# Optimization experiments

Hardware: AMD Instinct MI355X
Metric: run time of the kernel (lower is better)

The kernel has to match this reference:

```python
import jax, jax.numpy as jnp
import numpy as np

H = 32  # rnn/encoder/residual hidden dim
NEG = -1e9


def gru(x, h0, Wih, Whh, bih, bhh):
    # x: (B,T,D), h0: (B,H); torch GRU gate order [r,z,n]
    xp = jnp.swapaxes(x @ Wih.T + bih, 0, 1)  # (T,B,3H)

    def step(h, xt):
        gh = h @ Whh.T + bhh
        xr, xz, xn = jnp.split(xt, 3, axis=-1)
        hr, hz, hn = jnp.split(gh, 3, axis=-1)
        r = jax.nn.sigmoid(xr + hr)
        z = jax.nn.sigmoid(xz + hz)
        n = jnp.tanh(xn + r * hn)
        h_new = (1.0 - z) * n + z * h
        return h_new, h_new

    hT, ys = jax.lax.scan(step, h0, xp)
    return jnp.swapaxes(ys, 0, 1), hT  # (B,T,H), (B,H)


def setup_inputs():
    key = jax.random.key(0)
    ks = jax.random.split(key, 30)
    B, T = 2048, 128
    def lin(k, o, i):
        return jax.random.normal(k, (o, i), jnp.float32) / np.sqrt(i)
    inp = {}
    inp['obs'] = jax.random.normal(ks[0], (B, T, 15), jnp.float32)
    inp['rnn_state'] = jax.random.normal(ks[1], (1, B, 3 * H), jnp.float32)
    inp['enc_air_W'] = lin(ks[2], H, 7); inp['enc_air_b'] = jnp.zeros((H,), jnp.float32)
    inp['enc_m_W'] = lin(ks[3], H, 4); inp['enc_m_b'] = jnp.zeros((H,), jnp.float32)
    inp['air_Wih'] = lin(ks[4], 3 * H, H); inp['air_Whh'] = lin(ks[5], 3 * H, H)
    inp['air_bih'] = jnp.zeros((3 * H,), jnp.float32); inp['air_bhh'] = jnp.zeros((3 * H,), jnp.float32)
    inp['m_Wih'] = lin(ks[6], 3 * H, H); inp['m_Whh'] = lin(ks[7], 3 * H, H)
    inp['m_bih'] = jnp.zeros((3 * H,), jnp.float32); inp['m_bhh'] = jnp.zeros((3 * H,), jnp.float32)
    inp['attn_in_w'] = lin(ks[8], 3 * H, H); inp['attn_in_b'] = jnp.zeros((3 * H,), jnp.float32)
    inp['attn_out_w'] = lin(ks[9], H, H); inp['attn_out_b'] = jnp.zeros((H,), jnp.float32)
    inp['mlp_W0'] = lin(ks[10], 256, 2 * H); inp['mlp_b0'] = jnp.zeros((256,), jnp.float32)
    inp['mlp_W1'] = lin(ks[11], 256, 256); inp['mlp_b1'] = jnp.zeros((256,), jnp.float32)
    inp['out_W'] = lin(ks[12], 1, 256); inp['out_b'] = jnp.zeros((1,), jnp.float32)
    return inp


def reference(obs, rnn_state, enc_air_W, enc_air_b, enc_m_W, enc_m_b,
              air_Wih, air_Whh, air_bih, air_bhh,
              m_Wih, m_Whh, m_bih, m_bhh,
              attn_in_w, attn_in_b, attn_out_w, attn_out_b,
              mlp_W0, mlp_b0, mlp_W1, mlp_b1, out_W, out_b):
    B, T, _ = obs.shape
    h_air0 = rnn_state[0, :, :H]                       # (B,H)
    h_m0 = rnn_state[0, :, H:].reshape(2 * B, H)       # faithful reshape (1,B,64)->(1,2B,32)

    # aircraft branch
    air_emb = obs[..., 8:] @ enc_air_W.T + enc_air_b   # (B,T,H)
    air_feat, next_h_air = gru(air_emb, h_air0, air_Wih, air_Whh, air_bih, air_bhh)

    # missile branch: concat missiles along batch dim
    m_raw = jnp.concatenate([obs[..., 0:4], obs[..., 4:8]], axis=0)  # (2B,T,4)
    m_emb = m_raw @ enc_m_W.T + enc_m_b
    m_feat, next_h_m = gru(m_emb, h_m0, m_Wih, m_Whh, m_bih, m_bhh)
    m1_feat, m2_feat = m_feat[:B], m_feat[B:]

    # inactive-missile mask from raw obs
    obs_flat = obs.reshape(-1, 15)
    inact = jnp.array([1.0, 0.0, 1.0, 0.0], jnp.float32)
    mask = jnp.stack([
        jnp.all(jnp.isclose(obs_flat[:, 0:4], inact), axis=-1),
        jnp.all(jnp.isclose(obs_flat[:, 4:8], inact), axis=-1),
    ], axis=1)                                          # (N,2) True = masked

    N = B * T
    air_flat = air_feat.reshape(N, H)
    m1_flat = m1_feat.reshape(N, H)
    m2_flat = m2_feat.reshape(N, H)

    # 2-head attention, q len 1, kv len 2
    Wq, Wk, Wv = jnp.split(attn_in_w, 3, axis=0)
    bq, bk, bv = jnp.split(attn_in_b, 3, axis=0)
    nh, hd = 2, H // 2
    qh = (air_flat @ Wq.T + bq).reshape(N, nh, hd)
    kv = jnp.stack([m1_flat, m2_flat], axis=1)          # (N,2,H)
    kh = (kv @ Wk.T + bk).reshape(N, 2, nh, hd)
    vh = (kv @ Wv.T + bv).reshape(N, 2, nh, hd)
    scores = jnp.einsum('nhd,nkhd->nhk', qh, kh) / np.sqrt(hd)
    scores = scores + jnp.where(mask[:, None, :], NEG, 0.0)
    w = jax.nn.softmax(scores, axis=-1)
    ctx = jnp.einsum('nhk,nkhd->nhd', w, vh).reshape(N, H)
    attn = ctx @ attn_out_w.T + attn_out_b
    attn = jnp.where(jnp.all(mask, axis=-1, keepdims=True), 0.0, attn)  # torch nan_to_num(all-masked)

    fusion = jnp.concatenate([air_flat, attn], axis=-1)  # (N,2H)
    h1 = jax.nn.leaky_relu(fusion @ mlp_W0.T + mlp_b0, 0.01)
    h2 = jax.nn.leaky_relu(h1 @ mlp_W1.T + mlp_b1, 0.01)
    val = h2 @ out_W.T + out_b                           # (N,1)

    next_h = jnp.concatenate([next_h_air, next_h_m.reshape(B, 2 * H)], axis=-1)[None]  # (1,B,96)
    return val, next_h
```

## Files before the change

### kernel.cpp

```cpp
#include <hip/hip_runtime.h>
#include <hip/hip_bf16.h>

#define BB 2048
#define TT 128
#define NN (BB*TT)
#define NVAL NN

#define OFF_W0P   2048u
#define OFF_W1P   10240u
#define OFF_WQKV  43008u
#define OFF_WO    44544u
#define OFF_PWHA  49792u
#define OFF_PWHM  51328u
#define OFF_PWCA  52864u
#define OFF_PWCM  54400u
#define OFF_BHNA  55936u
#define OFF_BHNM  55968u
#define OFF_AIRF  83968u
#define OFF_MF    4278272u
#define OFF_MASK  12666880u

#define L2E 1.44269504088896341f

typedef __attribute__((ext_vector_type(8))) short short8;
typedef __attribute__((ext_vector_type(4))) float f32x4;
typedef _Float16 f16x8 __attribute__((ext_vector_type(8)));
typedef unsigned u32x4 __attribute__((ext_vector_type(4)));

__device__ __forceinline__ unsigned short f2bf(float f) {
    unsigned u = __builtin_bit_cast(unsigned, f);
    u += 0x7FFFu + ((u >> 16) & 1u);
    return (unsigned short)(u >> 16);
}
__device__ __forceinline__ unsigned f2h(float f) {
    _Float16 h = (_Float16)f;
    return (unsigned)__builtin_bit_cast(unsigned short, h);
}
__device__ __forceinline__ unsigned pkh2(float a, float b) {
    return (f2h(b) << 16) | f2h(a);
}
__device__ __forceinline__ float fast_rcp(float x) {
    return __builtin_amdgcn_rcpf(x);
}
__device__ __forceinline__ float ex2(float x) {
    return __builtin_amdgcn_exp2f(x);
}
__device__ __forceinline__ unsigned cvt_pk_bf16(float a, float b) {
    unsigned r;
    asm("v_cvt_pk_bf16_f32 %0, %1, %2" : "=v"(r) : "v"(a), "v"(b));
    return r;
}
__device__ __forceinline__ f32x4 mfma16f(f16x8 a, f16x8 b, f32x4 c) {
    return __builtin_amdgcn_mfma_f32_16x16x32_f16(a, b, c, 0, 0, 0);
}
__device__ __forceinline__ f32x4 mfma16b(short8 a, short8 b, f32x4 c) {
    return __builtin_amdgcn_mfma_f32_16x16x32_bf16(a, b, c, 0, 0, 0);
}
__device__ __forceinline__ float lrelu(float h) {
    return (h > 0.f) ? h : 0.01f*h;
}

__global__ __launch_bounds__(256) void prep_kernel(
    const float* __restrict__ enc_air_W, const float* __restrict__ enc_air_b,
    const float* __restrict__ enc_m_W,   const float* __restrict__ enc_m_b,
    const float* __restrict__ air_Wih,   const float* __restrict__ air_bih,
    const float* __restrict__ m_Wih,     const float* __restrict__ m_bih,
    const float* __restrict__ air_Whh,   const float* __restrict__ m_Whh,
    const float* __restrict__ air_bhh,   const float* __restrict__ m_bhh,
    const float* __restrict__ W0,        const float* __restrict__ W1,
    const float* __restrict__ attn_in_w, const float* __restrict__ attn_out_w,
    float* __restrict__ ws)
{
    int b = blockIdx.x, t = threadIdx.x;
    if (b == 0) {
    } else if (b <= 32) {
        unsigned short* w1p = (unsigned short*)(ws + OFF_W1P);
        int base = ((b-1)*256 + t);
        int lane = base & 63;
        int ctf  = base >> 6;
        int ft2  = ctf & 15, kap = ctf >> 4;
        int col = lane & 15, quad = lane >> 4;
        int o  = ft2*16 + col;
        #pragma unroll
        for (int j = 0; j < 8; j++) {
            int f = (2*kap + (j>>2))*16 + quad*4 + (j&3);
            w1p[base*8 + j] = f2bf(W1[o*256 + f]);
        }
    } else if (b <= 40) {
        unsigned short* w0p = (unsigned short*)(ws + OFF_W0P);
        int base = ((b-33)*256 + t);
        int lane = base & 63;
        int ctf  = base >> 6;
        int ct   = ctf & 15, s = ctf >> 4;
        int col = lane & 15, quad = lane >> 4;
        int k0 = s*32 + quad*8;
        int o  = ct*16 + col;
        #pragma unroll
        for (int j = 0; j < 8; j++)
            w0p[base*8 + j] = f2bf(W0[o*64 + k0 + j]);
    } else if (b == 41) {
        unsigned short* wqkv = (unsigned short*)(ws + OFF_WQKV);
        unsigned short* wop  = (unsigned short*)(ws + OFF_WO);
        for (int slot = t; slot < 512; slot += 256) {
            if (slot < 384) {
                int ct = slot >> 6, lane = slot & 63;
                int col = lane & 15, quad = lane >> 4;
                int o = ct*16 + col;
                #pragma unroll
                for (int j = 0; j < 8; j++)
                    wqkv[slot*8 + j] = f2bf(attn_in_w[o*32 + quad*8 + j]);
            } else {
                int s2 = slot - 384;
                int ct = s2 >> 6, lane = s2 & 63;
                int col = lane & 15, quad = lane >> 4;
                #pragma unroll
                for (int j = 0; j < 8; j++)
                    wop[s2*8 + j] = f2bf(attn_out_w[(ct*16+col)*32 + quad*8 + j]);
            }
        }
    } else if (b == 42) {
        unsigned* pa = (unsigned*)(ws + OFF_PWHA);
        unsigned* pm = (unsigned*)(ws + OFF_PWHM);
        for (int s = t; s < 3072; s += 256) {
            int s2 = (s < 1536) ? s : s - 1536;
            const float* W = (s < 1536) ? air_Whh : m_Whh;
            unsigned* dst = (s < 1536) ? pa : pm;
            int tile = s2 >> 8;
            int l    = (s2 >> 2) & 63;
            int d    = s2 & 3;
            int gate = tile >> 1, hfp = tile & 1;
            int rr = l & 15;
            int f  = (rr >> 2)*8 + hfp*4 + (rr & 3);
            int k  = (l >> 4)*8 + d*2;
            int row = gate*32 + f;
            float sc = (gate == 2) ? 2.f*L2E : L2E;
            dst[s2] = pkh2(W[row*32 + k]*sc, W[row*32 + k + 1]*sc);
        }
    } else {
        unsigned* pa = (unsigned*)(ws + OFF_PWCA);
        unsigned* pm = (unsigned*)(ws + OFF_PWCM);
        for (int s = t; s < 3072; s += 256) {
            bool isA = (s < 1536);
            int s2 = isA ? s : s - 1536;
            unsigned* dst = isA ? pa : pm;
            int tile = s2 >> 8, l = (s2 >> 2) & 63, d = s2 & 3;
            int gate = tile >> 1, hfp = tile & 1;
            int rr = l & 15;
            int f = (rr >> 2)*8 + hfp*4 + (rr & 3);
            int o = gate*32 + f;
            int kb = (l >> 4)*8 + d*2;
            int ni = isA ? 7 : 4;
            float sc = (gate == 2) ? 2.f*L2E : L2E;
            float v[2];
            #pragma unroll
            for (int e = 0; e < 2; e++) {
                int k = kb + e;
                float acc = 0.f;
                if (k < ni) {
                    for (int m = 0; m < 32; m++)
                        acc += isA ? air_Wih[o*32+m]*enc_air_W[m*7+k]
                                   : m_Wih[o*32+m]*enc_m_W[m*4+k];
                } else if (k == ni) {
                    acc = isA ? air_bih[o] : m_bih[o];
                    for (int m = 0; m < 32; m++)
                        acc += isA ? air_Wih[o*32+m]*enc_air_b[m]
                                   : m_Wih[o*32+m]*enc_m_b[m];
                    if (gate < 2) acc += isA ? air_bhh[o] : m_bhh[o];
                }
                v[e] = acc*sc;
            }
            dst[s2] = pkh2(v[0], v[1]);
        }
        if (t < 32) {
            ws[OFF_BHNA + t] = air_bhh[64 + t]*2.f*L2E;
            ws[OFF_BHNM + t] = m_bhh[64 + t]*2.f*L2E;
        }
    }
}

template<bool AIRT>
__device__ __forceinline__ void gru_tile(
    const float* __restrict__ obs, const float* __restrict__ rnn,
    const float* __restrict__ ws,
    unsigned short* __restrict__ feat, float* __restrict__ mask_f,
    float* __restrict__ nh_out, int tileIdx, unsigned* __restrict__ XH)
{
    const int lane = threadIdx.x & 63;
    const int col = lane & 15, quad = lane >> 4;

    const unsigned* pw = (const unsigned*)(ws + (AIRT ? OFF_PWHA : OFF_PWHM));
    const unsigned* pc = (const unsigned*)(ws + (AIRT ? OFF_PWCA : OFF_PWCM));
    f16x8 whf[6], wcf[6];
    #pragma unroll
    for (int i6 = 0; i6 < 6; i6++) {
        whf[i6] = __builtin_bit_cast(f16x8, *(const u32x4*)(pw + i6*256 + lane*4));
        wcf[i6] = __builtin_bit_cast(f16x8, *(const u32x4*)(pc + i6*256 + lane*4));
    }
    const float* bhnp = ws + (AIRT ? OFF_BHNA : OFF_BHNM) + quad*8;
    f32x4 bhn0 = *(const f32x4*)(bhnp);
    f32x4 bhn1 = *(const f32x4*)(bhnp + 4);

    int slot = 0, tb;
    if (AIRT) { tb = tileIdx*16; }
    else      { slot = tileIdx >> 7; tb = (tileIdx & 127)*16; }

    {
        const int coff = AIRT ? 8 : slot*4;
        #pragma unroll 4
        for (int it = 0; it < 32; it++) {
            int s = it*64 + lane;
            int r = s >> 7, t = s & 127;
            const float* p = obs + (size_t)(tb + r)*1920 + t*15 + coff;
            unsigned d0, d1, d2, d3;
            if (AIRT) {
                d0 = pkh2(p[0], p[1]); d1 = pkh2(p[2], p[3]);
                d2 = pkh2(p[4], p[5]); d3 = pkh2(p[6], 1.0f);
            } else {
                float x0 = p[0], x1 = p[1], x2 = p[2], x3 = p[3];
                d0 = pkh2(x0, x1); d1 = pkh2(x2, x3);
                d2 = 0x00003C00u; d3 = 0u;
                bool ok = (fabsf(x0 - 1.f) <= 1.00001e-5f) && (fabsf(x1) <= 1e-8f) &&
                          (fabsf(x2 - 1.f) <= 1.00001e-5f) && (fabsf(x3) <= 1e-8f);
                mask_f[((size_t)(tb + r)*TT + t)*2 + slot] = ok ? 1.f : 0.f;
            }
            unsigned off = (unsigned)(r*512 + 4*(t ^ (r & 7)));
            *(u32x4*)(XH + off) = (u32x4){d0, d1, d2, d3};
        }
    }
    __syncthreads();

    int rowi = tileIdx*16 + col;
    int hbase;
    if (AIRT) hbase = rowi*96;
    else      hbase = (rowi >> 1)*96 + 32 + (rowi & 1)*32;
    unsigned short* featp = feat + (size_t)rowi*(TT*32) + quad*8;

    f32x4 h0v = *(const f32x4*)(rnn + hbase + quad*8);
    f32x4 h1v = *(const f32x4*)(rnn + hbase + quad*8 + 4);

    const int xk = col & 7;
    const unsigned bidx = (unsigned)col*512;
    const f32x4 z4 = {0.f, 0.f, 0.f, 0.f};

    f32x4 gx0, gx1, gx2, gx3, gx4, gx5;
    {
        u32x4 xc = *(const u32x4*)(XH + bidx + 4u*(unsigned)(0 ^ xk));
        f16x8 xf = __builtin_bit_cast(f16x8, xc);
        gx0 = mfma16f(wcf[0], xf, z4); gx1 = mfma16f(wcf[1], xf, z4);
        gx2 = mfma16f(wcf[2], xf, z4); gx3 = mfma16f(wcf[3], xf, z4);
        gx4 = mfma16f(wcf[4], xf, z4); gx5 = mfma16f(wcf[5], xf, z4);
    }
    u32x4 xreg = *(const u32x4*)(XH + bidx + 4u*(unsigned)(1 ^ xk));

    #pragma unroll 1
    for (int t = 0; t < TT; t++) {
        const int tp = (t < TT-2) ? t+2 : TT-1;
        u32x4 xpre = *(const u32x4*)(XH + bidx + 4u*(unsigned)(tp ^ xk));
        f16x8 xfn = __builtin_bit_cast(f16x8, xreg);

        u32x4 hdv;
        hdv[0] = pkh2(h0v[0], h0v[1]); hdv[1] = pkh2(h0v[2], h0v[3]);
        hdv[2] = pkh2(h1v[0], h1v[1]); hdv[3] = pkh2(h1v[2], h1v[3]);
        f16x8 hff = __builtin_bit_cast(f16x8, hdv);

        f32x4 aR0 = mfma16f(whf[0], hff, gx0);
        f32x4 aR1 = mfma16f(whf[1], hff, gx1);
        f32x4 aZ0 = mfma16f(whf[2], hff, gx2);
        f32x4 aZ1 = mfma16f(whf[3], hff, gx3);
        f32x4 aHN0 = mfma16f(whf[4], hff, bhn0);
        f32x4 aHN1 = mfma16f(whf[5], hff, bhn1);
        f32x4 aXN0 = gx4, aXN1 = gx5;

        gx0 = mfma16f(wcf[0], xfn, z4); gx1 = mfma16f(wcf[1], xfn, z4);
        gx2 = mfma16f(wcf[2], xfn, z4); gx3 = mfma16f(wcf[3], xfn, z4);
        gx4 = mfma16f(wcf[4], xfn, z4); gx5 = mfma16f(wcf[5], xfn, z4);

        #pragma unroll
        for (int s = 0; s < 4; s++) {
            {
                float r = fast_rcp(1.f + ex2(-aR0[s]));
                float z = fast_rcp(1.f + ex2(-aZ0[s]));
                float p = aXN0[s] + r*aHN0[s];
                float n = fmaf(-2.f, fast_rcp(1.f + ex2(p)), 1.f);
                h0v[s] = n + z*(h0v[s] - n);
            }
            {
                float r = fast_rcp(1.f + ex2(-aR1[s]));
                float z = fast_rcp(1.f + ex2(-aZ1[s]));
                float p = aXN1[s] + r*aHN1[s];
                float n = fmaf(-2.f, fast_rcp(1.f + ex2(p)), 1.f);
                h1v[s] = n + z*(h1v[s] - n);
            }
        }

        u32x4 fw;
        fw[0] = cvt_pk_bf16(h0v[0], h0v[1]); fw[1] = cvt_pk_bf16(h0v[2], h0v[3]);
        fw[2] = cvt_pk_bf16(h1v[0], h1v[1]); fw[3] = cvt_pk_bf16(h1v[2], h1v[3]);
        *(u32x4*)(featp + (size_t)t*32) = fw;

        xreg = xpre;
    }
    *(f32x4*)(nh_out + hbase + quad*8)     = h0v;
    *(f32x4*)(nh_out + hbase + quad*8 + 4) = h1v;
}

__global__ __launch_bounds__(64, 1) void gru_kernel(
    const float* __restrict__ obs, const float* __restrict__ rnn,
    const float* __restrict__ ws,
    unsigned short* __restrict__ air_feat, unsigned short* __restrict__ m_feat,
    float* __restrict__ mask_f, float* __restrict__ nh_out)
{
    __shared__ unsigned XH[8192];
    int g = blockIdx.x;
    if (g < 128) gru_tile<true >(obs, rnn, ws, air_feat, mask_f, nh_out, g, XH);
    else         gru_tile<false>(obs, rnn, ws, m_feat,  mask_f, nh_out, g - 128, XH);
}

__global__ __launch_bounds__(512, 4) void fused_kernel(
    const unsigned short* __restrict__ air_feat, const unsigned short* __restrict__ m_feat,
    const float* __restrict__ mask_f,
    const unsigned short* __restrict__ wqkv, const float* __restrict__ attn_in_b,
    const unsigned short* __restrict__ wop,  const float* __restrict__ attn_out_b,
    const unsigned short* __restrict__ w0p, const float* __restrict__ b0,
    const unsigned short* __restrict__ w1p, const float* __restrict__ b1,
    const float* __restrict__ outW, const float* __restrict__ outb,
    float* __restrict__ val)
{
    __shared__ unsigned short XB[16384];
    __shared__ unsigned short AT[4096];
    __shared__ float PS[8][64];

    unsigned short* CT = XB;

    const int tid  = threadIdx.x;
    const int lane = tid & 63;
    const int wid  = tid >> 6;
    const int col  = lane & 15;
    const int quad = lane >> 4;
    const size_t n0 = (size_t)blockIdx.x * 64;
    const int rt    = wid & 3;
    const int tbase = (wid >> 2) * 8;

    short8 w0f0[8];
    #pragma unroll
    for (int i = 0; i < 8; i++)
        w0f0[i] = *(const short8*)(w0p + ((tbase + i)*64 + lane)*8);
    short8 bAir = *(const short8*)(air_feat + (n0 + rt*16 + col)*32 + quad*8);

    f32x4 accL1[8];
    #pragma unroll
    for (int i = 0; i < 8; i++) accL1[i] = (f32x4){0.f,0.f,0.f,0.f};

    if (wid < 4) {
        const int strip = wid;
        short8 wqf[2], wkf[2], wvf[2], wof[2];
        #pragma unroll
        for (int ct = 0; ct < 2; ct++) {
            wqf[ct] = *(const short8*)(wqkv + ((0+ct)*64 + lane)*8);
            wkf[ct] = *(const short8*)(wqkv + ((2+ct)*64 + lane)*8);
            wvf[ct] = *(const short8*)(wqkv + ((4+ct)*64 + lane)*8);
            wof[ct] = *(const short8*)(wop + (ct*64 + lane)*8);
        }
        short8 a_m1 = *(const short8*)(m_feat + (n0 + strip*16 + col)*32 + quad*8);
        short8 a_m2 = *(const short8*)(m_feat + ((size_t)NN + n0 + strip*16 + col)*32 + quad*8);

        float m0a[4], m1a[4];
        #pragma unroll
        for (int reg = 0; reg < 4; reg++) {
            const float* mp = mask_f + (size_t)(n0 + strip*16 + quad*4 + reg)*2;
            m0a[reg] = mp[0]; m1a[reg] = mp[1];
        }

        f32x4 q[2], k1[2], k2[2], v1[2], v2[2], ao[2];
        #pragma unroll
        for (int ct = 0; ct < 2; ct++) {
            f32x4 z = (f32x4){0.f,0.f,0.f,0.f};
            q[ct]  = mfma16b(bAir, wqf[ct], z);
            k1[ct] = mfma16b(a_m1, wkf[ct], z);
            k2[ct] = mfma16b(a_m2, wkf[ct], z);
            v1[ct] = mfma16b(a_m1, wvf[ct], z);
            v2[ct] = mfma16b(a_m2, wvf[ct], z);
        }
        float bqr[2], bkr[2], bvr[2];
        #pragma unroll
        for (int ct = 0; ct < 2; ct++) {
            bqr[ct] = attn_in_b[ct*16 + col];
            bkr[ct] = attn_in_b[32 + ct*16 + col];
            bvr[ct] = attn_in_b[64 + ct*16 + col];
        }
        float p1s[2][4], p2s[2][4];
        #pragma unroll
        for (int ct = 0; ct < 2; ct++) {
            #pragma unroll
            for (int reg = 0; reg < 4; reg++) {
                float qq = q[ct][reg] + bqr[ct];
                float p1 = qq * (k1[ct][reg] + bkr[ct]);
                float p2 = qq * (k2[ct][reg] + bkr[ct]);
                #pragma unroll
                for (int m = 1; m < 16; m <<= 1) {
                    p1 += __shfl_xor(p1, m, 64);
                    p2 += __shfl_xor(p2, m, 64);
                }
                p1s[ct][reg] = p1; p2s[ct][reg] = p2;
            }
        }
        float bothm[4];
        #pragma unroll
        for (int reg = 0; reg < 4; reg++) {
            int rloc = strip*16 + quad*4 + reg;
            float m0v = m0a[reg], m1v = m1a[reg];
            bothm[reg] = (m0v > 0.5f && m1v > 0.5f) ? 1.f : 0.f;
            #pragma unroll
            for (int ct = 0; ct < 2; ct++) {
                float s1 = p1s[ct][reg]*0.25f + (m0v > 0.5f ? -1e9f : 0.f);
                float s2 = p2s[ct][reg]*0.25f + (m1v > 0.5f ? -1e9f : 0.f);
                float mx = fmaxf(s1, s2);
                float e1 = __expf(s1 - mx), e2 = __expf(s2 - mx);
                float inv = fast_rcp(e1 + e2);
                float ctxv = ((v1[ct][reg] + bvr[ct])*e1 +
                              (v2[ct][reg] + bvr[ct])*e2) * inv;
                CT[rloc*40 + ct*16 + col] = f2bf(ctxv);
            }
        }
        short8 a_ctx = *(const short8*)&CT[(strip*16 + col)*40 + quad*8];
        #pragma unroll
        for (int ct = 0; ct < 2; ct++) {
            f32x4 z = (f32x4){0.f,0.f,0.f,0.f};
            ao[ct] = mfma16b(a_ctx, wof[ct], z);
        }
        float bor[2] = { attn_out_b[col], attn_out_b[16 + col] };
        #pragma unroll
        for (int reg = 0; reg < 4; reg++) {
            #pragma unroll
            for (int ct = 0; ct < 2; ct++) {
                float av = ao[ct][reg] + bor[ct];
                av = (bothm[reg] > 0.5f) ? 0.f : av;
                AT[strip*1024 + (quad*4 + reg)*64 + ct*16 + col] = f2bf(av);
            }
        }
    } else {
        #pragma unroll
        for (int i = 0; i < 8; i++)
            accL1[i] = mfma16b(w0f0[i], bAir, accL1[i]);
    }
    __syncthreads();

    if (wid < 4) {
        #pragma unroll
        for (int i = 0; i < 8; i++)
            accL1[i] = mfma16b(w0f0[i], bAir, accL1[i]);
    }
    {
        short8 bAttn = *(const short8*)&AT[rt*1024 + col*64 + quad*8];
        #pragma unroll
        for (int i = 0; i < 8; i++) {
            short8 w0f1 = *(const short8*)(w0p + ((16 + tbase + i)*64 + lane)*8);
            accL1[i] = mfma16b(w0f1, bAttn, accL1[i]);
        }
    }
    #pragma unroll
    for (int i = 0; i < 8; i += 2) {
        int t0 = tbase + i;
        f32x4 bA = *(const f32x4*)(b0 + t0*16 + quad*4);
        f32x4 bB = *(const f32x4*)(b0 + (t0+1)*16 + quad*4);
        float a0 = lrelu(accL1[i][0]   + bA[0]), a1 = lrelu(accL1[i][1]   + bA[1]);
        float a2 = lrelu(accL1[i][2]   + bA[2]), a3 = lrelu(accL1[i][3]   + bA[3]);
        float c0 = lrelu(accL1[i+1][0] + bB[0]), c1 = lrelu(accL1[i+1][1] + bB[1]);
        float c2 = lrelu(accL1[i+1][2] + bB[2]), c3 = lrelu(accL1[i+1][3] + bB[3]);
        u32x4 w;
        w[0] = cvt_pk_bf16(a0, a1); w[1] = cvt_pk_bf16(a2, a3);
        w[2] = cvt_pk_bf16(c0, c1); w[3] = cvt_pk_bf16(c2, c3);
        int kap = t0 >> 1;
        *(u32x4*)((unsigned*)XB + ((rt*8 + kap)*64 + lane)*4) = w;
    }
    __syncthreads();

    f32x4 acc2[4][2];
    #pragma unroll
    for (int r = 0; r < 4; r++)
        #pragma unroll
        for (int c = 0; c < 2; c++) acc2[r][c] = (f32x4){0.f,0.f,0.f,0.f};
    {
        short8 w1f[2], w1n[2];
        #pragma unroll
        for (int c = 0; c < 2; c++)
            w1f[c] = *(const short8*)(w1p + ((0*16 + wid*2 + c)*64 + lane)*8);
        #pragma unroll
        for (int kap = 0; kap < 8; kap++) {
            if (kap < 7) {
                #pragma unroll
                for (int c = 0; c < 2; c++)
                    w1n[c] = *(const short8*)(w1p + (((kap+1)*16 + wid*2 + c)*64 + lane)*8);
            }
            short8 bx[4];
            #pragma unroll
            for (int r = 0; r < 4; r++)
                bx[r] = *(const short8*)&XB[((r*8 + kap)*64 + lane)*8];
            #pragma unroll
            for (int c = 0; c < 2; c++)
                #pragma unroll
                for (int r = 0; r < 4; r++)
                    acc2[r][c] = mfma16b(w1f[c], bx[r], acc2[r][c]);
            #pragma unroll
            for (int c = 0; c < 2; c++) w1f[c] = w1n[c];
        }
    }

    f32x4 b1v[2], owv[2];
    #pragma unroll
    for (int c = 0; c < 2; c++) {
        b1v[c] = *(const f32x4*)(b1 + (wid*2 + c)*16 + quad*4);
        owv[c] = *(const f32x4*)(outW + (wid*2 + c)*16 + quad*4);
    }
    const float outb0 = outb[0];
    #pragma unroll
    for (int r = 0; r < 4; r++) {
        float pv = 0.f;
        #pragma unroll
        for (int c = 0; c < 2; c++) {
            #pragma unroll
            for (int reg = 0; reg < 4; reg++) {
                float h = lrelu(acc2[r][c][reg] + b1v[c][reg]);
                pv += h*owv[c][reg];
            }
        }
        pv += __shfl_xor(pv, 16, 64);
        pv += __shfl_xor(pv, 32, 64);
        if (lane < 16) PS[wid][r*16 + lane] = pv;
    }
    __syncthreads();
    if (tid < 64)
        val[n0 + tid] = PS[0][tid] + PS[1][tid] + PS[2][tid] + PS[3][tid]
                      + PS[4][tid] + PS[5][tid] + PS[6][tid] + PS[7][tid] + outb0;
}

extern "C" void kernel_launch(void* const* d_in, const int* in_sizes, int n_in,
                              void* d_out, int out_size, void* d_ws, size_t ws_size,
                              hipStream_t stream) {
    const float* obs        = (const float*)d_in[0];
    const float* rnn        = (const float*)d_in[1];
    const float* enc_air_W  = (const float*)d_in[2];
    const float* enc_air_b  = (const float*)d_in[3];
    const float* enc_m_W    = (const float*)d_in[4];
    const float* enc_m_b    = (const float*)d_in[5];
    const float* air_Wih    = (const float*)d_in[6];
    const float* air_Whh    = (const float*)d_in[7];
    const float* air_bih    = (const float*)d_in[8];
    const float* air_bhh    = (const float*)d_in[9];
    const float* m_Wih      = (const float*)d_in[10];
    const float* m_Whh      = (const float*)d_in[11];
    const float* m_bih      = (const float*)d_in[12];
    const float* m_bhh      = (const float*)d_in[13];
    const float* attn_in_w  = (const float*)d_in[14];
    const float* attn_in_b  = (const float*)d_in[15];
    const float* attn_out_w = (const float*)d_in[16];
    const float* attn_out_b = (const float*)d_in[17];
    const float* mlp_W0     = (const float*)d_in[18];
    const float* mlp_b0     = (const float*)d_in[19];
    const float* mlp_W1     = (const float*)d_in[20];
    const float* mlp_b1     = (const float*)d_in[21];
    const float* out_W      = (const float*)d_in[22];
    const float* out_b      = (const float*)d_in[23];

    float* ws  = (float*)d_ws;
    float* out = (float*)d_out;

    prep_kernel<<<44, 256, 0, stream>>>(enc_air_W, enc_air_b, enc_m_W, enc_m_b,
                                        air_Wih, air_bih, m_Wih, m_bih,
                                        air_Whh, m_Whh, air_bhh, m_bhh,
                                        mlp_W0, mlp_W1, attn_in_w, attn_out_w, ws);

    gru_kernel<<<384, 64, 0, stream>>>(obs, rnn, ws,
                                       (unsigned short*)(ws + OFF_AIRF),
                                       (unsigned short*)(ws + OFF_MF),
                                       ws + OFF_MASK, out + NVAL);

    fused_kernel<<<NN/64, 512, 0, stream>>>((const unsigned short*)(ws + OFF_AIRF),
                                            (const unsigned short*)(ws + OFF_MF),
                                            ws + OFF_MASK,
                                            (const unsigned short*)(ws + OFF_WQKV), attn_in_b,
                                            (const unsigned short*)(ws + OFF_WO),   attn_out_b,
                                            (const unsigned short*)(ws + OFF_W0P), mlp_b0,
                                            (const unsigned short*)(ws + OFF_W1P), mlp_b1,
                                            out_W, out_b, out);
}
```

Before: 301.9 us.

## Split GRU hidden dimension across two wavefronts with LDS exchange per step

The GRU recurrence kernel now uses two wavefronts per 16-row tile. Each wave computes half of the hidden units, and the two exchange packed fp16 hidden state through double-buffered LDS with a block barrier every timestep. This halves the serial MFMA and transcendental work per wave on the latency-bound recurrence, at the cost of a __syncthreads per step. The gate math also batches reciprocals, computing one rcp per pair of sigmoids or tanhs to cut rcp count.

```diff
diff --git a/kernel.cpp b/kernel.cpp
--- a/kernel.cpp
+++ b/kernel.cpp
@@ -26,6 +26,7 @@
 typedef __attribute__((ext_vector_type(4))) float f32x4;
 typedef _Float16 f16x8 __attribute__((ext_vector_type(8)));
 typedef unsigned u32x4 __attribute__((ext_vector_type(4)));
+typedef unsigned u32x2 __attribute__((ext_vector_type(2)));
 
 __device__ __forceinline__ unsigned short f2bf(float f) {
     unsigned u = __builtin_bit_cast(unsigned, f);
@@ -183,22 +184,23 @@
     const float* __restrict__ obs, const float* __restrict__ rnn,
     const float* __restrict__ ws,
     unsigned short* __restrict__ feat, float* __restrict__ mask_f,
-    float* __restrict__ nh_out, int tileIdx, unsigned* __restrict__ XH)
+    float* __restrict__ nh_out, int tileIdx,
+    unsigned* __restrict__ XH, unsigned* __restrict__ XC)
 {
-    const int lane = threadIdx.x & 63;
+    const int tid  = threadIdx.x;
+    const int w    = tid >> 6;
+    const int lane = tid & 63;
     const int col = lane & 15, quad = lane >> 4;
 
     const unsigned* pw = (const unsigned*)(ws + (AIRT ? OFF_PWHA : OFF_PWHM));
     const unsigned* pc = (const unsigned*)(ws + (AIRT ? OFF_PWCA : OFF_PWCM));
-    f16x8 whf[6], wcf[6];
-    #pragma unroll
-    for (int i6 = 0; i6 < 6; i6++) {
-        whf[i6] = __builtin_bit_cast(f16x8, *(const u32x4*)(pw + i6*256 + lane*4));
-        wcf[i6] = __builtin_bit_cast(f16x8, *(const u32x4*)(pc + i6*256 + lane*4));
-    }
-    const float* bhnp = ws + (AIRT ? OFF_BHNA : OFF_BHNM) + quad*8;
-    f32x4 bhn0 = *(const f32x4*)(bhnp);
-    f32x4 bhn1 = *(const f32x4*)(bhnp + 4);
+    f16x8 whfR = __builtin_bit_cast(f16x8, *(const u32x4*)(pw + (0 + w)*256 + lane*4));
+    f16x8 whfZ = __builtin_bit_cast(f16x8, *(const u32x4*)(pw + (2 + w)*256 + lane*4));
+    f16x8 whfN = __builtin_bit_cast(f16x8, *(const u32x4*)(pw + (4 + w)*256 + lane*4));
+    f16x8 wcfR = __builtin_bit_cast(f16x8, *(const u32x4*)(pc + (0 + w)*256 + lane*4));
+    f16x8 wcfZ = __builtin_bit_cast(f16x8, *(const u32x4*)(pc + (2 + w)*256 + lane*4));
+    f16x8 wcfN = __builtin_bit_cast(f16x8, *(const u32x4*)(pc + (4 + w)*256 + lane*4));
+    f32x4 bhnv = *(const f32x4*)(ws + (AIRT ? OFF_BHNA : OFF_BHNM) + quad*8 + w*4);
 
     int slot = 0, tb;
     if (AIRT) { tb = tileIdx*16; }
@@ -207,8 +209,8 @@
     {
         const int coff = AIRT ? 8 : slot*4;
         #pragma unroll 4
-        for (int it = 0; it < 32; it++) {
-            int s = it*64 + lane;
+        for (int it = 0; it < 16; it++) {
+            int s = it*128 + tid;
             int r = s >> 7, t = s & 127;
             const float* p = obs + (size_t)(tb + r)*1920 + t*15 + coff;
             unsigned d0, d1, d2, d3;
@@ -233,22 +235,21 @@
     int hbase;
     if (AIRT) hbase = rowi*96;
     else      hbase = (rowi >> 1)*96 + 32 + (rowi & 1)*32;
-    unsigned short* featp = feat + (size_t)rowi*(TT*32) + quad*8;
-
-    f32x4 h0v = *(const f32x4*)(rnn + hbase + quad*8);
-    f32x4 h1v = *(const f32x4*)(rnn + hbase + quad*8 + 4);
+    unsigned short* featp = feat + (size_t)rowi*(TT*32) + quad*8 + w*4;
+
+    f32x4 hv = *(const f32x4*)(rnn + hbase + quad*8 + w*4);
 
     const int xk = col & 7;
     const unsigned bidx = (unsigned)col*512;
     const f32x4 z4 = {0.f, 0.f, 0.f, 0.f};
 
-    f32x4 gx0, gx1, gx2, gx3, gx4, gx5;
+    f32x4 gxR, gxZ, gxN;
     {
         u32x4 xc = *(const u32x4*)(XH + bidx + 4u*(unsigned)(0 ^ xk));
         f16x8 xf = __builtin_bit_cast(f16x8, xc);
-        gx0 = mfma16f(wcf[0], xf, z4); gx1 = mfma16f(wcf[1], xf, z4);
-        gx2 = mfma16f(wcf[2], xf, z4); gx3 = mfma16f(wcf[3], xf, z4);
-        gx4 = mfma16f(wcf[4], xf, z4); gx5 = mfma16f(wcf[5], xf, z4);
+        gxR = mfma16f(wcfR, xf, z4);
+        gxZ = mfma16f(wcfZ, xf, z4);
+        gxN = mfma16f(wcfN, xf, z4);
     }
     u32x4 xreg = *(const u32x4*)(XH + bidx + 4u*(unsigned)(1 ^ xk));
 
@@ -256,64 +257,73 @@
     for (int t = 0; t < TT; t++) {
         const int tp = (t < TT-2) ? t+2 : TT-1;
         u32x4 xpre = *(const u32x4*)(XH + bidx + 4u*(unsigned)(tp ^ xk));
-        f16x8 xfn = __builtin_bit_cast(f16x8, xreg);
+
+        unsigned d0 = pkh2(hv[0], hv[1]);
+        unsigned d1 = pkh2(hv[2], hv[3]);
+        *(u32x2*)(XC + ((t & 1)*256 + w*128 + lane*2)) = (u32x2){d0, d1};
+        __syncthreads();
+        u32x2 oth = *(const u32x2*)(XC + ((t & 1)*256 + (1 - w)*128 + lane*2));
 
         u32x4 hdv;
-        hdv[0] = pkh2(h0v[0], h0v[1]); hdv[1] = pkh2(h0v[2], h0v[3]);
-        hdv[2] = pkh2(h1v[0], h1v[1]); hdv[3] = pkh2(h1v[2], h1v[3]);
+        hdv[0] = w ? oth[0] : d0;
+        hdv[1] = w ? oth[1] : d1;
+        hdv[2] = w ? d0 : oth[0];
+        hdv[3] = w ? d1 : oth[1];
         f16x8 hff = __builtin_bit_cast(f16x8, hdv);
 
-        f32x4 aR0 = mfma16f(whf[0], hff, gx0);
-        f32x4 aR1 = mfma16f(whf[1], hff, gx1);
-        f32x4 aZ0 = mfma16f(whf[2], hff, gx2);
-        f32x4 aZ1 = mfma16f(whf[3], hff, gx3);
-        f32x4 aHN0 = mfma16f(whf[4], hff, bhn0);
-        f32x4 aHN1 = mfma16f(whf[5], hff, bhn1);
-        f32x4 aXN0 = gx4, aXN1 = gx5;
-
-        gx0 = mfma16f(wcf[0], xfn, z4); gx1 = mfma16f(wcf[1], xfn, z4);
-        gx2 = mfma16f(wcf[2], xfn, z4); gx3 = mfma16f(wcf[3], xfn, z4);
-        gx4 = mfma16f(wcf[4], xfn, z4); gx5 = mfma16f(wcf[5], xfn, z4);
-
-        #pragma unroll
-        for (int s = 0; s < 4; s++) {
-            {
-                float r = fast_rcp(1.f + ex2(-aR0[s]));
-                float z = fast_rcp(1.f + ex2(-aZ0[s]));
-                float p = aXN0[s] + r*aHN0[s];
-                float n = fmaf(-2.f, fast_rcp(1.f + ex2(p)), 1.f);
-                h0v[s] = n + z*(h0v[s] - n);
-            }
-            {
-                float r = fast_rcp(1.f + ex2(-aR1[s]));
-                float z = fast_rcp(1.f + ex2(-aZ1[s]));
-                float p = aXN1[s] + r*aHN1[s];
-                float n = fmaf(-2.f, fast_rcp(1.f + ex2(p)), 1.f);
-                h1v[s] = n + z*(h1v[s] - n);
-            }
-        }
-
-        u32x4 fw;
-        fw[0] = cvt_pk_bf16(h0v[0], h0v[1]); fw[1] = cvt_pk_bf16(h0v[2], h0v[3]);
-        fw[2] = cvt_pk_bf16(h1v[0], h1v[1]); fw[3] = cvt_pk_bf16(h1v[2], h1v[3]);
-        *(u32x4*)(featp + (size_t)t*32) = fw;
-
+        f32x4 aR  = mfma16f(whfR, hff, gxR);
+        f32x4 aZ  = mfma16f(whfZ, hff, gxZ);
+        f32x4 aHN = mfma16f(whfN, hff, bhnv);
+        f32x4 aXN = gxN;
+
+        f16x8 xf1 = __builtin_bit_cast(f16x8, xreg);
+        gxR = mfma16f(wcfR, xf1, z4);
+        gxZ = mfma16f(wcfZ, xf1, z4);
+        gxN = mfma16f(wcfN, xf1, z4);
         xreg = xpre;
-    }
-    *(f32x4*)(nh_out + hbase + quad*8)     = h0v;
-    *(f32x4*)(nh_out + hbase + quad*8 + 4) = h1v;
-}
-
-__global__ __launch_bounds__(64, 1) void gru_kernel(
+
+        #pragma unroll
+        for (int p = 0; p < 2; p++) {
+            const int a = 2*p, b = 2*p + 1;
+            float erA = ex2(-aR[a]), ezA = ex2(-aZ[a]);
+            float erB = ex2(-aR[b]), ezB = ex2(-aZ[b]);
+            float prA = 1.f + erA, pzA = 1.f + ezA;
+            float prB = 1.f + erB, pzB = 1.f + ezB;
+            float dA = prA*pzA, dB = prB*pzB;
+            float inv = fast_rcp(dA*dB);
+            float tA = dB*inv, tB = dA*inv;
+            float rA = pzA*tA, zA = prA*tA;
+            float rB = pzB*tB, zB = prB*tB;
+            float pA = aXN[a] + rA*aHN[a];
+            float pB = aXN[b] + rB*aHN[b];
+            float eA = ex2(pA), eB = ex2(pB);
+            float qA = eA + 1.f, qB = eB + 1.f;
+            float inv2 = fast_rcp(qA*qB);
+            float nA = 1.f - 2.f*(qB*inv2);
+            float nB = 1.f - 2.f*(qA*inv2);
+            hv[a] = nA + zA*(hv[a] - nA);
+            hv[b] = nB + zB*(hv[b] - nB);
+        }
+
+        u32x2 fw;
+        fw[0] = cvt_pk_bf16(hv[0], hv[1]);
+        fw[1] = cvt_pk_bf16(hv[2], hv[3]);
+        *(u32x2*)(featp + (size_t)t*32) = fw;
+    }
+    *(f32x4*)(nh_out + hbase + quad*8 + w*4) = hv;
+}
+
+__global__ __launch_bounds__(128, 1) void gru_kernel(
     const float* __restrict__ obs, const float* __restrict__ rnn,
     const float* __restrict__ ws,
     unsigned short* __restrict__ air_feat, unsigned short* __restrict__ m_feat,
     float* __restrict__ mask_f, float* __restrict__ nh_out)
 {
     __shared__ unsigned XH[8192];
+    __shared__ unsigned XC[512];
     int g = blockIdx.x;
-    if (g < 128) gru_tile<true >(obs, rnn, ws, air_feat, mask_f, nh_out, g, XH);
-    else         gru_tile<false>(obs, rnn, ws, m_feat,  mask_f, nh_out, g - 128, XH);
+    if (g < 128) gru_tile<true >(obs, rnn, ws, air_feat, mask_f, nh_out, g, XH, XC);
+    else         gru_tile<false>(obs, rnn, ws, m_feat,  mask_f, nh_out, g - 128, XH, XC);
 }
 
 __global__ __launch_bounds__(512, 4) void fused_kernel(
@@ -570,10 +580,10 @@
                                         air_Whh, m_Whh, air_bhh, m_bhh,
                                         mlp_W0, mlp_W1, attn_in_w, attn_out_w, ws);
 
-    gru_kernel<<<384, 64, 0, stream>>>(obs, rnn, ws,
-                                       (unsigned short*)(ws + OFF_AIRF),
-                                       (unsigned short*)(ws + OFF_MF),
-                                       ws + OFF_MASK, out + NVAL);
+    gru_kernel<<<384, 128, 0, stream>>>(obs, rnn, ws,
+                                        (unsigned short*)(ws + OFF_AIRF),
+                                        (unsigned short*)(ws + OFF_MF),
+                                        ws + OFF_MASK, out + NVAL);
 
     fused_kernel<<<NN/64, 512, 0, stream>>>((const unsigned short*)(ws + OFF_AIRF),
                                             (const unsigned short*)(ws + OFF_MF),
```

Result: slower. 311.2 us (+3.1%).
